# Kernel tuning notes

Hardware: AMD Instinct MI355X
Metric: run time of the kernel (lower is better)

The kernel has to match this reference:

```python
import jax, jax.numpy as jnp
import numpy as np

C = 512
NUM_HEADS = 8
HEAD_DIM = 64
GROUPS = 32
EPS = 1e-5


def setup_inputs() -> dict:
    key = jax.random.key(0)
    ks = jax.random.split(key, 7)
    x = jax.random.normal(ks[0], (2, C, 64, 64), dtype=jnp.float32)
    norm_w = jnp.ones((C,), jnp.float32)
    norm_b = jnp.zeros((C,), jnp.float32)
    s1 = 1.0 / np.sqrt(C)
    qkv_w = jax.random.uniform(ks[1], (3 * C, C), jnp.float32, -s1, s1)
    qkv_b = jax.random.uniform(ks[2], (3 * C,), jnp.float32, -s1, s1)
    proj_w = jax.random.uniform(ks[3], (C, C), jnp.float32, -s1, s1)
    proj_b = jax.random.uniform(ks[4], (C,), jnp.float32, -s1, s1)
    return {"x": x, "norm_w": norm_w, "norm_b": norm_b,
            "qkv_w": qkv_w, "qkv_b": qkv_b,
            "proj_w": proj_w, "proj_b": proj_b}


def reference(x, norm_w, norm_b, qkv_w, qkv_b, proj_w, proj_b):
    b, c, h, w = x.shape
    n = h * w
    x_flat = x.reshape(b, c, n)
    # GroupNorm(32, C): stats over (channels-in-group, spatial)
    xg = x_flat.reshape(b, GROUPS, c // GROUPS, n)
    mean = xg.mean(axis=(2, 3), keepdims=True)
    var = xg.var(axis=(2, 3), keepdims=True)
    hn = ((xg - mean) * jax.lax.rsqrt(var + EPS)).reshape(b, c, n)
    hn = hn * norm_w[None, :, None] + norm_b[None, :, None]
    # 1x1 conv QKV = matmul over channel dim
    qkv = jnp.einsum('oc,bcn->bon', qkv_w, hn) + qkv_b[None, :, None]
    q, k, v = jnp.split(qkv, 3, axis=1)
    q = q.reshape(b, NUM_HEADS, HEAD_DIM, n)
    k = k.reshape(b, NUM_HEADS, HEAD_DIM, n)
    v = v.reshape(b, NUM_HEADS, HEAD_DIM, n)
    scale = HEAD_DIM ** (-0.5)
    attn = jnp.einsum('bhdn,bhdm->bhnm', q, k) * scale  # [b,H,N,N]
    attn = jax.nn.softmax(attn, axis=-1)
    out = jnp.einsum('bhnm,bhdm->bhdn', attn, v).reshape(b, c, n)
    out = jnp.einsum('oc,bcn->bon', proj_w, out) + proj_b[None, :, None]
    return (x_flat + out).reshape(b, c, h, w)
```

## Files before the change

### kernel.cpp

```cpp
#include <hip/hip_runtime.h>
#include <hip/hip_bf16.h>
#include <math.h>

#define BATCH 2
#define CCH   512
#define NSP   4096
#define NHEAD 8
#define HDIM  64
#define NGRP  32
#define CPG   16
#define EPSV  1e-5f
#define NSPLIT 2
#define MTN   (NSP / NSPLIT / 64)
#define SMSCALE 0.1803368801111204f

typedef __attribute__((ext_vector_type(8))) short short8;
typedef __attribute__((ext_vector_type(4))) short short4v;
typedef __attribute__((ext_vector_type(4))) float f32x4;
typedef __hip_bfloat16 bf16;

static __device__ __forceinline__ unsigned pk2(float a, float b) {
    return ((__float_as_uint(a) + 0x8000u) >> 16) |
           ((__float_as_uint(b) + 0x8000u) & 0xFFFF0000u);
}
static __device__ __forceinline__ unsigned pk1(float a) {
    return (__float_as_uint(a) + 0x8000u) >> 16;
}
static __device__ __forceinline__ float upk(unsigned u) {
    unsigned v = u << 16;
    return __uint_as_float(v);
}
static __device__ __forceinline__ float fexp2(float x) {
    return __builtin_amdgcn_exp2f(x);
}
static __device__ __forceinline__ void gload16(const bf16* g, bf16* l) {
    __builtin_amdgcn_global_load_lds(
        (const __attribute__((address_space(1))) unsigned*)g,
        (__attribute__((address_space(3))) unsigned*)l, 16, 0, 0);
}

__global__ __launch_bounds__(256) void prep0(const float* __restrict__ x,
                                             const float* __restrict__ qkvw,
                                             const float* __restrict__ pw,
                                             float* __restrict__ stats,
                                             bf16* __restrict__ wq, bf16* __restrict__ wp) {
    if (blockIdx.x < 64) {
        const int bg = blockIdx.x;
        const float4* p = (const float4*)(x + (size_t)bg * (CPG * NSP));
        float s = 0.f, ss = 0.f;
        for (int i = threadIdx.x; i < CPG * NSP / 4; i += 256) {
            float4 v = p[i];
            s  += v.x + v.y + v.z + v.w;
            ss += v.x * v.x + v.y * v.y + v.z * v.z + v.w * v.w;
        }
        for (int o = 32; o > 0; o >>= 1) {
            s  += __shfl_down(s, o);
            ss += __shfl_down(ss, o);
        }
        __shared__ float shs[4], shss[4];
        const int wid = threadIdx.x >> 6, lane = threadIdx.x & 63;
        if (lane == 0) { shs[wid] = s; shss[wid] = ss; }
        __syncthreads();
        if (threadIdx.x == 0) {
            s  = shs[0] + shs[1] + shs[2] + shs[3];
            ss = shss[0] + shss[1] + shss[2] + shss[3];
            const float inv = 1.f / (float)(CPG * NSP);
            float mu  = s * inv;
            float var = ss * inv - mu * mu;
            stats[bg]      = mu;
            stats[64 + bg] = rsqrtf(var + EPSV);
        }
    } else {
        const int i = (blockIdx.x - 64) * 256 + threadIdx.x;
        const int NQ = 1536 * 512 / 4;
        float4 v; bf16* dst; int di;
        if (i < NQ) { v = ((const float4*)qkvw)[i]; dst = wq; di = i; }
        else        { v = ((const float4*)pw)[i - NQ]; dst = wp; di = i - NQ; }
        uint2 o = {pk2(v.x, v.y), pk2(v.z, v.w)};
        *(uint2*)(dst + (size_t)di * 4) = o;
    }
}

__global__ __launch_bounds__(256) void gn_apply_t(const float* __restrict__ x,
                                                  const float* __restrict__ stats,
                                                  const float* __restrict__ nw,
                                                  const float* __restrict__ nb,
                                                  bf16* __restrict__ hnt) {
    __shared__ float Ls[64][68];
    const int b  = blockIdx.z;
    const int c0 = blockIdx.y * 64;
    const int n0 = blockIdx.x * 64;
    const int t  = threadIdx.x;
    const int cl = t >> 4, n4 = (t & 15) * 4;
#pragma unroll
    for (int ph = 0; ph < 4; ph++) {
        const int c  = c0 + ph * 16 + cl;
        const int bg = b * NGRP + (c >> 4);
        const float mu = stats[bg], rs = stats[64 + bg];
        const float sw = nw[c] * rs;
        const float sb = nb[c] - mu * sw;
        float4 v = *(const float4*)&x[((size_t)b * CCH + c) * NSP + n0 + n4];
        float4 o;
        o.x = v.x * sw + sb; o.y = v.y * sw + sb;
        o.z = v.z * sw + sb; o.w = v.w * sw + sb;
        *(float4*)&Ls[ph * 16 + cl][n4] = o;
    }
    __syncthreads();
#pragma unroll
    for (int ph = 0; ph < 2; ph++) {
        const int task = ph * 256 + t;
        const int nl = task & 63, cc = (task >> 6) * 8;
        uint4 o;
        o.x = pk2(Ls[cc + 0][nl], Ls[cc + 1][nl]);
        o.y = pk2(Ls[cc + 2][nl], Ls[cc + 3][nl]);
        o.z = pk2(Ls[cc + 4][nl], Ls[cc + 5][nl]);
        o.w = pk2(Ls[cc + 6][nl], Ls[cc + 7][nl]);
        *(uint4*)&hnt[((size_t)b * NSP + n0 + nl) * CCH + c0 + cc] = o;
    }
}

#define GEMM_STAGE(CUR)                                         \
    gload16(aSrc0, &As[CUR][(wave * 16) * 32]);                 \
    gload16(aSrc1, &As[CUR][(64 + wave * 16) * 32]);            \
    gload16(bSrc0, &Bs[CUR][(wave * 16) * 32]);                 \
    gload16(bSrc1, &Bs[CUR][(64 + wave * 16) * 32]);            \
    aSrc0 += 32; aSrc1 += 32; bSrc0 += 32; bSrc1 += 32;

#define GEMM_MAIN(Wptr, Xptr)                                                            \
    __shared__ __align__(16) bf16 As[2][128 * 32];                                       \
    __shared__ __align__(16) bf16 Bs[2][128 * 32];                                       \
    const int t = threadIdx.x, wave = t >> 6, lane = t & 63;                             \
    const int quad = lane >> 4, l15 = lane & 15;                                         \
    const int srow = lane >> 2, scol = (lane & 3) * 8;                                   \
    const int b   = blockIdx.z;                                                          \
    const int wm = wave >> 1, wn = wave & 1;                                             \
    const int m0w = blockIdx.y * 128 + wm * 64;                                          \
    const int n0w = blockIdx.x * 128 + wn * 64;                                          \
    const bf16* aSrc0 = Wptr + (size_t)(blockIdx.y * 128 + wave * 16 + srow) * 512 + scol; \
    const bf16* aSrc1 = aSrc0 + (size_t)64 * 512;                                        \
    const bf16* bSrc0 = Xptr + ((size_t)b * NSP + blockIdx.x * 128 + wave * 16 + srow) * 512 + scol; \
    const bf16* bSrc1 = bSrc0 + (size_t)64 * 512;                                        \
    f32x4 acc[4][4];                                                                     \
    _Pragma("unroll")                                                                    \
    for (int i = 0; i < 4; i++)                                                          \
        _Pragma("unroll")                                                                \
        for (int j = 0; j < 4; j++) acc[i][j] = (f32x4){0.f, 0.f, 0.f, 0.f};             \
    GEMM_STAGE(0)                                                                        \
    __syncthreads();                                                                     \
    _Pragma("unroll")                                                                    \
    for (int ks = 0; ks < 16; ks++) {                                                    \
        const int cur = ks & 1;                                                          \
        if (ks < 15) { GEMM_STAGE(cur ^ 1) }                                             \
        short8 af[4], bfr[4];                                                            \
        _Pragma("unroll")                                                                \
        for (int mf = 0; mf < 4; mf++)                                                   \
            af[mf] = *(const short8*)&As[cur][(wm * 64 + mf * 16 + l15) * 32 + quad * 8]; \
        _Pragma("unroll")                                                                \
        for (int nf = 0; nf < 4; nf++)                                                   \
            bfr[nf] = *(const short8*)&Bs[cur][(wn * 64 + nf * 16 + l15) * 32 + quad * 8]; \
        _Pragma("unroll")                                                                \
        for (int mf = 0; mf < 4; mf++)                                                   \
            _Pragma("unroll")                                                            \
            for (int nf = 0; nf < 4; nf++)                                               \
                acc[mf][nf] = __builtin_amdgcn_mfma_f32_16x16x32_bf16(af[mf], bfr[nf],   \
                                                                      acc[mf][nf], 0, 0, 0); \
        __syncthreads();                                                                 \
    }

__global__ __launch_bounds__(256) void gemm_qkv(const bf16* __restrict__ Wb,
                                                const bf16* __restrict__ Xt,
                                                const float* __restrict__ bias,
                                                bf16* __restrict__ qt, bf16* __restrict__ kt,
                                                bf16* __restrict__ vt) {
    GEMM_MAIN(Wb, Xt)

    const int sec = m0w >> 9, h = (m0w >> 6) & 7, bh = b * NHEAD + h;
    const float sm = (sec == 0) ? SMSCALE : 1.0f;
    float bi[4][4];
#pragma unroll
    for (int mf = 0; mf < 4; mf++)
#pragma unroll
        for (int r = 0; r < 4; r++) bi[mf][r] = bias[m0w + mf * 16 + quad * 4 + r];

    if (sec < 2) {
        bf16* dst = (sec == 0) ? qt : kt;
#pragma unroll
        for (int mf = 0; mf < 4; mf++)
#pragma unroll
            for (int nf = 0; nf < 4; nf++) {
                const int n = n0w + nf * 16 + l15;
                float v0 = (acc[mf][nf][0] + bi[mf][0]) * sm;
                float v1 = (acc[mf][nf][1] + bi[mf][1]) * sm;
                float v2 = (acc[mf][nf][2] + bi[mf][2]) * sm;
                float v3 = (acc[mf][nf][3] + bi[mf][3]) * sm;
                uint2 o = {pk2(v0, v1), pk2(v2, v3)};
                *(uint2*)(dst + ((size_t)bh * NSP + n) * HDIM + mf * 16 + quad * 4) = o;
            }
    } else {
#pragma unroll
        for (int mf = 0; mf < 4; mf++)
#pragma unroll
            for (int nf = 0; nf < 4; nf++)
#pragma unroll
                for (int r = 0; r < 4; r++) {
                    const float v = acc[mf][nf][r] + bi[mf][r];
                    const int n = n0w + nf * 16 + l15;
                    const int d = mf * 16 + quad * 4 + r;
                    unsigned u = pk1(v);
                    vt[((size_t)bh * HDIM + d) * NSP + n] = *(bf16*)&u;
                }
    }
}

__global__ __launch_bounds__(256) void gemm_proj(const bf16* __restrict__ Wb,
                                                 const bf16* __restrict__ Xt,
                                                 const float* __restrict__ bias,
                                                 const float* __restrict__ resid,
                                                 float* __restrict__ out) {
    GEMM_MAIN(Wb, Xt)

    float bi[4][4];
#pragma unroll
    for (int mf = 0; mf < 4; mf++)
#pragma unroll
        for (int r = 0; r < 4; r++) bi[mf][r] = bias[m0w + mf * 16 + quad * 4 + r];
#pragma unroll
    for (int mf = 0; mf < 4; mf++)
#pragma unroll
        for (int nf = 0; nf < 4; nf++)
#pragma unroll
            for (int r = 0; r < 4; r++) {
                const int m = m0w + mf * 16 + quad * 4 + r;
                const int n = n0w + nf * 16 + l15;
                const size_t idx = ((size_t)b * CCH + m) * NSP + n;
                out[idx] = acc[mf][nf][r] + bi[mf][r] + resid[idx];
            }
}

__global__ __launch_bounds__(256, 2) void attn10(const bf16* __restrict__ qt,
                                                 const bf16* __restrict__ kt,
                                                 const bf16* __restrict__ vt,
                                                 bf16* __restrict__ opart,
                                                 float* __restrict__ lpart) {
    __shared__ __align__(16) bf16 Ks[64][68];
    __shared__ __align__(16) bf16 Vs[64][68];
    const int t = threadIdx.x, wave = t >> 6, lane = t & 63;
    const int quad = lane >> 4, l15 = lane & 15;
    const int blk = blockIdx.x;
    const int xcd = blk & 7, slot = blk >> 3;
    const int qtile = slot & 15;
    const int grp = xcd + 8 * (slot >> 4);
    const int spl = grp & 1, bh = grp >> 1;
    const int b = bh >> 3, h = bh & 7;
    const int qb  = qtile * 256 + wave * 64;
    const int kb0 = spl * (NSP / NSPLIT);

    const bf16* Qb = qt + (size_t)bh * NSP * HDIM;

    const int trow = t >> 3;
    const int tcol = (t & 7) * 8;
    const bf16* kSrcA = kt + (size_t)bh * NSP * HDIM + (size_t)(kb0 + trow) * HDIM + tcol;
    const bf16* kSrcB = kSrcA + 32 * HDIM;
    const bf16* vSrcA = vt + (size_t)bh * HDIM * NSP + (size_t)trow * NSP + kb0 + tcol;
    const bf16* vSrcB = vSrcA + (size_t)32 * NSP;
    bf16* kDstA = &Ks[trow][tcol];
    bf16* kDstB = &Ks[32 + trow][tcol];
    bf16* vDstA = &Vs[trow][tcol];
    bf16* vDstB = &Vs[32 + trow][tcol];

    short8 qf[4][2];
#pragma unroll
    for (int qs = 0; qs < 4; qs++)
#pragma unroll
        for (int c = 0; c < 2; c++)
            qf[qs][c] = *(const short8*)(Qb + (size_t)(qb + qs * 16 + l15) * HDIM + c * 32 + quad * 8);

    short8 onesf;
    {
        const short one = (short)0x3F80;
        short8 o1 = {one, one, one, one, one, one, one, one};
        short8 zz = {0, 0, 0, 0, 0, 0, 0, 0};
        onesf = (l15 == 0) ? o1 : zz;
    }

    f32x4 o[4][4], ol[4];
#pragma unroll
    for (int qs = 0; qs < 4; qs++) {
        ol[qs] = (f32x4){0.f, 0.f, 0.f, 0.f};
#pragma unroll
        for (int ds = 0; ds < 4; ds++) o[qs][ds] = (f32x4){0.f, 0.f, 0.f, 0.f};
    }

    uint4 rKA = *(const uint4*)kSrcA; kSrcA += 64 * HDIM;
    uint4 rKB = *(const uint4*)kSrcB; kSrcB += 64 * HDIM;
    uint4 rVA = *(const uint4*)vSrcA; vSrcA += 64;
    uint4 rVB = *(const uint4*)vSrcB; vSrcB += 64;

    for (int mt = 0; mt < MTN; mt++) {
        __syncthreads();
        *(uint4*)kDstA = rKA;
        *(uint4*)kDstB = rKB;
        *(uint4*)vDstA = rVA;
        *(uint4*)vDstB = rVB;
        __syncthreads();

        rKA = *(const uint4*)kSrcA; kSrcA += 64 * HDIM;
        rKB = *(const uint4*)kSrcB; kSrcB += 64 * HDIM;
        rVA = *(const uint4*)vSrcA; vSrcA += 64;
        rVB = *(const uint4*)vSrcB; vSrcB += 64;

        short8 kf[4][2], vf[4][2];
#pragma unroll
        for (int ms = 0; ms < 4; ms++)
#pragma unroll
            for (int c = 0; c < 2; c++)
                kf[ms][c] = *(const short8*)&Ks[ms * 16 + l15][c * 32 + quad * 8];
#pragma unroll
        for (int ds = 0; ds < 4; ds++)
#pragma unroll
            for (int c = 0; c < 2; c++)
                vf[ds][c] = *(const short8*)&Vs[ds * 16 + l15][c * 32 + quad * 8];

#pragma unroll
        for (int qs = 0; qs < 4; qs++) {
            f32x4 s[4];
            __builtin_amdgcn_s_setprio(1);
#pragma unroll
            for (int ms = 0; ms < 4; ms++) {
                f32x4 a = (f32x4){0.f, 0.f, 0.f, 0.f};
                a = __builtin_amdgcn_mfma_f32_16x16x32_bf16(kf[ms][0], qf[qs][0], a, 0, 0, 0);
                a = __builtin_amdgcn_mfma_f32_16x16x32_bf16(kf[ms][1], qf[qs][1], a, 0, 0, 0);
                s[ms] = a;
            }
            __builtin_amdgcn_s_setprio(0);

            unsigned rr[4][2];
#pragma unroll
            for (int ms = 0; ms < 4; ms++) {
                float e0 = fexp2(s[ms][0]);
                float e1 = fexp2(s[ms][1]);
                float e2 = fexp2(s[ms][2]);
                float e3 = fexp2(s[ms][3]);
                asm("v_cvt_pk_bf16_f32 %0, %1, %2" : "=v"(rr[ms][0]) : "v"(e0), "v"(e1));
                asm("v_cvt_pk_bf16_f32 %0, %1, %2" : "=v"(rr[ms][1]) : "v"(e2), "v"(e3));
            }
#pragma unroll
            for (int j = 0; j < 2; j++) {
                asm("v_permlane32_swap_b32 %0, %1" : "+v"(rr[0][j]), "+v"(rr[1][j]));
                asm("v_permlane32_swap_b32 %0, %1" : "+v"(rr[2][j]), "+v"(rr[3][j]));
            }
#pragma unroll
            for (int j = 0; j < 2; j++) {
                asm("v_permlane16_swap_b32 %0, %1" : "+v"(rr[0][j]), "+v"(rr[1][j]));
                asm("v_permlane16_swap_b32 %0, %1" : "+v"(rr[2][j]), "+v"(rr[3][j]));
            }
            short8 pf0, pf1;
            {
                unsigned* p0 = (unsigned*)&pf0;
                p0[0] = rr[0][0]; p0[1] = rr[0][1]; p0[2] = rr[1][0]; p0[3] = rr[1][1];
                unsigned* p1 = (unsigned*)&pf1;
                p1[0] = rr[2][0]; p1[1] = rr[2][1]; p1[2] = rr[3][0]; p1[3] = rr[3][1];
            }

            __builtin_amdgcn_s_setprio(1);
#pragma unroll
            for (int ds = 0; ds < 4; ds++) {
                f32x4 a = o[qs][ds];
                a = __builtin_amdgcn_mfma_f32_16x16x32_bf16(pf0, vf[ds][0], a, 0, 0, 0);
                a = __builtin_amdgcn_mfma_f32_16x16x32_bf16(pf1, vf[ds][1], a, 0, 0, 0);
                o[qs][ds] = a;
            }
            {
                f32x4 a = ol[qs];
                a = __builtin_amdgcn_mfma_f32_16x16x32_bf16(pf0, onesf, a, 0, 0, 0);
                a = __builtin_amdgcn_mfma_f32_16x16x32_bf16(pf1, onesf, a, 0, 0, 0);
                ol[qs] = a;
            }
            __builtin_amdgcn_s_setprio(0);
        }
    }

#pragma unroll
    for (int qs = 0; qs < 4; qs++) {
#pragma unroll
        for (int ds = 0; ds < 4; ds++)
#pragma unroll
            for (int r = 0; r < 4; r++) {
                const int q = qb + qs * 16 + quad * 4 + r;
                unsigned u = pk1(o[qs][ds][r]);
                opart[((size_t)(spl * BATCH + b) * NSP + q) * CCH + h * 64 + ds * 16 + l15] =
                    *(bf16*)&u;
            }
        if (l15 == 0) {
#pragma unroll
            for (int r = 0; r < 4; r++) {
                const int q = qb + qs * 16 + quad * 4 + r;
                lpart[(((size_t)spl * BATCH + b) * NHEAD + h) * NSP + q] = ol[qs][r];
            }
        }
    }
}

__global__ __launch_bounds__(256) void attn_combine(const bf16* __restrict__ opart,
                                                    const float* __restrict__ lpart,
                                                    bf16* __restrict__ att_t) {
    const int idx = blockIdx.x * 256 + threadIdx.x;
    const int c8 = (idx & 63) * 8;
    const int n  = (idx >> 6) & 4095;
    const int b  = idx >> 18;
    const int h  = c8 >> 6;
    float l = 0.f;
#pragma unroll
    for (int s = 0; s < NSPLIT; s++)
        l += lpart[(((size_t)s * BATCH + b) * NHEAD + h) * NSP + n];
    const float inv = 1.f / l;
    float acc[8] = {};
#pragma unroll
    for (int s = 0; s < NSPLIT; s++) {
        uint4 u = *(const uint4*)&opart[((size_t)(s * BATCH + b) * NSP + n) * CCH + c8];
        acc[0] += upk(u.x); acc[1] += upk(u.x >> 16);
        acc[2] += upk(u.y); acc[3] += upk(u.y >> 16);
        acc[4] += upk(u.z); acc[5] += upk(u.z >> 16);
        acc[6] += upk(u.w); acc[7] += upk(u.w >> 16);
    }
    uint4 o;
    o.x = pk2(acc[0] * inv, acc[1] * inv);
    o.y = pk2(acc[2] * inv, acc[3] * inv);
    o.z = pk2(acc[4] * inv, acc[5] * inv);
    o.w = pk2(acc[6] * inv, acc[7] * inv);
    *(uint4*)&att_t[((size_t)b * NSP + n) * CCH + c8] = o;
}

extern "C" void kernel_launch(void* const* d_in, const int* in_sizes, int n_in,
                              void* d_out, int out_size, void* d_ws, size_t ws_size,
                              hipStream_t stream) {
    const float* x    = (const float*)d_in[0];
    const float* nw   = (const float*)d_in[1];
    const float* nb   = (const float*)d_in[2];
    const float* qkvw = (const float*)d_in[3];
    const float* qkvb = (const float*)d_in[4];
    const float* pw   = (const float*)d_in[5];
    const float* pb   = (const float*)d_in[6];
    float* out = (float*)d_out;
    char* ws   = (char*)d_ws;

    float* stats = (float*)ws;
    bf16* wq  = (bf16*)(ws + (size_t)1  * 1024 * 1024);
    bf16* wp  = (bf16*)(ws + (size_t)3  * 1024 * 1024);
    bf16* hnt = (bf16*)(ws + (size_t)4  * 1024 * 1024);
    bf16* qtb = (bf16*)(ws + (size_t)12 * 1024 * 1024);
    bf16* ktb = (bf16*)(ws + (size_t)20 * 1024 * 1024);
    bf16* vtb = (bf16*)(ws + (size_t)28 * 1024 * 1024);
    bf16* opart = (bf16*)(ws + (size_t)36 * 1024 * 1024);
    float* lpart = (float*)(ws + (size_t)56 * 1024 * 1024);
    bf16* att = hnt;

    hipLaunchKernelGGL(prep0, dim3(64 + 1024), dim3(256), 0, stream,
                       x, qkvw, pw, stats, wq, wp);
    hipLaunchKernelGGL(gn_apply_t, dim3(NSP / 64, CCH / 64, BATCH), dim3(256), 0, stream,
                       x, stats, nw, nb, hnt);
    hipLaunchKernelGGL(gemm_qkv, dim3(NSP / 128, 1536 / 128, BATCH), dim3(256), 0, stream,
                       wq, hnt, qkvb, qtb, ktb, vtb);
    hipLaunchKernelGGL(attn10, dim3(512), dim3(256), 0, stream,
                       qtb, ktb, vtb, opart, lpart);
    hipLaunchKernelGGL(attn_combine, dim3(BATCH * NSP * CCH / 8 / 256), dim3(256), 0, stream,
                       opart, lpart, att);
    hipLaunchKernelGGL(gemm_proj, dim3(NSP / 128, CCH / 128, BATCH), dim3(256), 0, stream,
                       wp, att, pb, x, out);
}
```

Measured before the change: 222.8 us.

## Drop split-K attention and combine kernel; use 128-thread blocks over full key range

Removes the two-way key split and the separate combine kernel, so each attention block walks all 4096 keys and normalizes its output by the row sum before writing bf16 directly. Blocks shrink to two waves (128 query rows), so the grid stays at 512 blocks, and each thread now loads four K and four V rows per tile. This removes the partial-output write and reread, the combine launch, and the bf16 rounding of partial sums. In exchange, each block's serial loop is twice as long and fewer waves share each K/V tile load.

```diff
diff --git a/kernel.cpp b/kernel.cpp
--- a/kernel.cpp
+++ b/kernel.cpp
@@ -10,8 +10,7 @@
 #define NGRP  32
 #define CPG   16
 #define EPSV  1e-5f
-#define NSPLIT 2
-#define MTN   (NSP / NSPLIT / 64)
+#define MTN   (NSP / 64)
 #define SMSCALE 0.1803368801111204f
 
 typedef __attribute__((ext_vector_type(8))) short short8;
@@ -237,36 +236,35 @@
             }
 }
 
-__global__ __launch_bounds__(256, 2) void attn10(const bf16* __restrict__ qt,
+__global__ __launch_bounds__(128, 2) void attn10(const bf16* __restrict__ qt,
                                                  const bf16* __restrict__ kt,
                                                  const bf16* __restrict__ vt,
-                                                 bf16* __restrict__ opart,
-                                                 float* __restrict__ lpart) {
+                                                 bf16* __restrict__ att) {
     __shared__ __align__(16) bf16 Ks[64][68];
     __shared__ __align__(16) bf16 Vs[64][68];
     const int t = threadIdx.x, wave = t >> 6, lane = t & 63;
     const int quad = lane >> 4, l15 = lane & 15;
     const int blk = blockIdx.x;
     const int xcd = blk & 7, slot = blk >> 3;
-    const int qtile = slot & 15;
-    const int grp = xcd + 8 * (slot >> 4);
-    const int spl = grp & 1, bh = grp >> 1;
+    const int qtile = slot & 31;
+    const int bh = xcd + 8 * (slot >> 5);
     const int b = bh >> 3, h = bh & 7;
-    const int qb  = qtile * 256 + wave * 64;
-    const int kb0 = spl * (NSP / NSPLIT);
+    const int qb  = qtile * 128 + wave * 64;
 
     const bf16* Qb = qt + (size_t)bh * NSP * HDIM;
 
     const int trow = t >> 3;
     const int tcol = (t & 7) * 8;
-    const bf16* kSrcA = kt + (size_t)bh * NSP * HDIM + (size_t)(kb0 + trow) * HDIM + tcol;
-    const bf16* kSrcB = kSrcA + 32 * HDIM;
-    const bf16* vSrcA = vt + (size_t)bh * HDIM * NSP + (size_t)trow * NSP + kb0 + tcol;
-    const bf16* vSrcB = vSrcA + (size_t)32 * NSP;
-    bf16* kDstA = &Ks[trow][tcol];
-    bf16* kDstB = &Ks[32 + trow][tcol];
-    bf16* vDstA = &Vs[trow][tcol];
-    bf16* vDstB = &Vs[32 + trow][tcol];
+    const bf16* kS = kt + (size_t)bh * NSP * HDIM + (size_t)trow * HDIM + tcol;
+    const bf16* vS = vt + (size_t)bh * HDIM * NSP + (size_t)trow * NSP + tcol;
+    bf16* kD0 = &Ks[trow +  0][tcol];
+    bf16* kD1 = &Ks[trow + 16][tcol];
+    bf16* kD2 = &Ks[trow + 32][tcol];
+    bf16* kD3 = &Ks[trow + 48][tcol];
+    bf16* vD0 = &Vs[trow +  0][tcol];
+    bf16* vD1 = &Vs[trow + 16][tcol];
+    bf16* vD2 = &Vs[trow + 32][tcol];
+    bf16* vD3 = &Vs[trow + 48][tcol];
 
     short8 qf[4][2];
 #pragma unroll
@@ -291,23 +289,39 @@
         for (int ds = 0; ds < 4; ds++) o[qs][ds] = (f32x4){0.f, 0.f, 0.f, 0.f};
     }
 
-    uint4 rKA = *(const uint4*)kSrcA; kSrcA += 64 * HDIM;
-    uint4 rKB = *(const uint4*)kSrcB; kSrcB += 64 * HDIM;
-    uint4 rVA = *(const uint4*)vSrcA; vSrcA += 64;
-    uint4 rVB = *(const uint4*)vSrcB; vSrcB += 64;
+    uint4 rK0 = *(const uint4*)(kS +  0 * 16 * HDIM);
+    uint4 rK1 = *(const uint4*)(kS +  1 * 16 * HDIM);
+    uint4 rK2 = *(const uint4*)(kS +  2 * 16 * HDIM);
+    uint4 rK3 = *(const uint4*)(kS +  3 * 16 * HDIM);
+    uint4 rV0 = *(const uint4*)(vS + (size_t) 0 * 16 * NSP);
+    uint4 rV1 = *(const uint4*)(vS + (size_t) 1 * 16 * NSP);
+    uint4 rV2 = *(const uint4*)(vS + (size_t) 2 * 16 * NSP);
+    uint4 rV3 = *(const uint4*)(vS + (size_t) 3 * 16 * NSP);
+    kS += 64 * HDIM;
+    vS += 64;
 
     for (int mt = 0; mt < MTN; mt++) {
         __syncthreads();
-        *(uint4*)kDstA = rKA;
-        *(uint4*)kDstB = rKB;
-        *(uint4*)vDstA = rVA;
-        *(uint4*)vDstB = rVB;
+        *(uint4*)kD0 = rK0;
+        *(uint4*)kD1 = rK1;
+        *(uint4*)kD2 = rK2;
+        *(uint4*)kD3 = rK3;
+        *(uint4*)vD0 = rV0;
+        *(uint4*)vD1 = rV1;
+        *(uint4*)vD2 = rV2;
+        *(uint4*)vD3 = rV3;
         __syncthreads();
 
-        rKA = *(const uint4*)kSrcA; kSrcA += 64 * HDIM;
-        rKB = *(const uint4*)kSrcB; kSrcB += 64 * HDIM;
-        rVA = *(const uint4*)vSrcA; vSrcA += 64;
-        rVB = *(const uint4*)vSrcB; vSrcB += 64;
+        rK0 = *(const uint4*)(kS +  0 * 16 * HDIM);
+        rK1 = *(const uint4*)(kS +  1 * 16 * HDIM);
+        rK2 = *(const uint4*)(kS +  2 * 16 * HDIM);
+        rK3 = *(const uint4*)(kS +  3 * 16 * HDIM);
+        rV0 = *(const uint4*)(vS + (size_t) 0 * 16 * NSP);
+        rV1 = *(const uint4*)(vS + (size_t) 1 * 16 * NSP);
+        rV2 = *(const uint4*)(vS + (size_t) 2 * 16 * NSP);
+        rV3 = *(const uint4*)(vS + (size_t) 3 * 16 * NSP);
+        kS += 64 * HDIM;
+        vS += 64;
 
         short8 kf[4][2], vf[4][2];
 #pragma unroll
@@ -382,53 +396,19 @@
 
 #pragma unroll
     for (int qs = 0; qs < 4; qs++) {
+        float inv[4];
+#pragma unroll
+        for (int r = 0; r < 4; r++)
+            inv[r] = 1.0f / __shfl(ol[qs][r], lane & 48);
 #pragma unroll
         for (int ds = 0; ds < 4; ds++)
 #pragma unroll
             for (int r = 0; r < 4; r++) {
                 const int q = qb + qs * 16 + quad * 4 + r;
-                unsigned u = pk1(o[qs][ds][r]);
-                opart[((size_t)(spl * BATCH + b) * NSP + q) * CCH + h * 64 + ds * 16 + l15] =
-                    *(bf16*)&u;
-            }
-        if (l15 == 0) {
-#pragma unroll
-            for (int r = 0; r < 4; r++) {
-                const int q = qb + qs * 16 + quad * 4 + r;
-                lpart[(((size_t)spl * BATCH + b) * NHEAD + h) * NSP + q] = ol[qs][r];
-            }
-        }
-    }
-}
-
-__global__ __launch_bounds__(256) void attn_combine(const bf16* __restrict__ opart,
-                                                    const float* __restrict__ lpart,
-                                                    bf16* __restrict__ att_t) {
-    const int idx = blockIdx.x * 256 + threadIdx.x;
-    const int c8 = (idx & 63) * 8;
-    const int n  = (idx >> 6) & 4095;
-    const int b  = idx >> 18;
-    const int h  = c8 >> 6;
-    float l = 0.f;
-#pragma unroll
-    for (int s = 0; s < NSPLIT; s++)
-        l += lpart[(((size_t)s * BATCH + b) * NHEAD + h) * NSP + n];
-    const float inv = 1.f / l;
-    float acc[8] = {};
-#pragma unroll
-    for (int s = 0; s < NSPLIT; s++) {
-        uint4 u = *(const uint4*)&opart[((size_t)(s * BATCH + b) * NSP + n) * CCH + c8];
-        acc[0] += upk(u.x); acc[1] += upk(u.x >> 16);
-        acc[2] += upk(u.y); acc[3] += upk(u.y >> 16);
-        acc[4] += upk(u.z); acc[5] += upk(u.z >> 16);
-        acc[6] += upk(u.w); acc[7] += upk(u.w >> 16);
-    }
-    uint4 o;
-    o.x = pk2(acc[0] * inv, acc[1] * inv);
-    o.y = pk2(acc[2] * inv, acc[3] * inv);
-    o.z = pk2(acc[4] * inv, acc[5] * inv);
-    o.w = pk2(acc[6] * inv, acc[7] * inv);
-    *(uint4*)&att_t[((size_t)b * NSP + n) * CCH + c8] = o;
+                unsigned u = pk1(o[qs][ds][r] * inv[r]);
+                att[((size_t)b * NSP + q) * CCH + h * 64 + ds * 16 + l15] = *(bf16*)&u;
+            }
+    }
 }
 
 extern "C" void kernel_launch(void* const* d_in, const int* in_sizes, int n_in,
@@ -451,8 +431,6 @@
     bf16* qtb = (bf16*)(ws + (size_t)12 * 1024 * 1024);
     bf16* ktb = (bf16*)(ws + (size_t)20 * 1024 * 1024);
     bf16* vtb = (bf16*)(ws + (size_t)28 * 1024 * 1024);
-    bf16* opart = (bf16*)(ws + (size_t)36 * 1024 * 1024);
-    float* lpart = (float*)(ws + (size_t)56 * 1024 * 1024);
     bf16* att = hnt;
 
     hipLaunchKernelGGL(prep0, dim3(64 + 1024), dim3(256), 0, stream,
@@ -461,10 +439,8 @@
                        x, stats, nw, nb, hnt);
     hipLaunchKernelGGL(gemm_qkv, dim3(NSP / 128, 1536 / 128, BATCH), dim3(256), 0, stream,
                        wq, hnt, qkvb, qtb, ktb, vtb);
-    hipLaunchKernelGGL(attn10, dim3(512), dim3(256), 0, stream,
-                       qtb, ktb, vtb, opart, lpart);
-    hipLaunchKernelGGL(attn_combine, dim3(BATCH * NSP * CCH / 8 / 256), dim3(256), 0, stream,
-                       opart, lpart, att);
+    hipLaunchKernelGGL(attn10, dim3(512), dim3(128), 0, stream,
+                       qtb, ktb, vtb, att);
     hipLaunchKernelGGL(gemm_proj, dim3(NSP / 128, CCH / 128, BATCH), dim3(256), 0, stream,
                        wp, att, pb, x, out);
 }
```

New measurement: 279.1 us. 25.3% more time.
